# Kernel tuning notes

Hardware: AMD Instinct MI355X
Metric: run time of the kernel (lower is better)

Reference implementation:

```python
import jax, jax.numpy as jnp
import numpy as np

K = 100  # sliding-window size hard-coded in the original forward


def setup_inputs() -> dict:
    key = jax.random.key(0)
    x = jax.random.normal(key, (32, 1, 1124, 1124), dtype=jnp.float32)
    return {"x": x}


def reference(x):
    # Sliding 100x100 mean over every stride-1 patch (gq == patch mean),
    # computed via a 2D integral image (summed-area table) so we never
    # materialize the [B, C, outH, outW, K, K] patch tensor.
    B, C, H, W = x.shape
    s = jnp.cumsum(jnp.cumsum(x, axis=2), axis=3)
    # pad one zero row/col at the front -> S has shape [B, C, H+1, W+1]
    S = jnp.pad(s, ((0, 0), (0, 0), (1, 0), (1, 0)))
    sums = (S[:, :, K:, K:] - S[:, :, :-K, K:]
            - S[:, :, K:, :-K] + S[:, :, :-K, :-K])  # [B, C, H-K+1, W-K+1]
    # gq averages over the whole patch (all channels + spatial) -> 1 channel out
    out = jnp.sum(sums, axis=1, keepdims=True) / jnp.asarray(K * K * C, x.dtype)
    return out  # [B, 1, H-99, W-99]
```

## Files before the change

### kernel.cpp

```cpp
#include <hip/hip_runtime.h>


#define H_IN    1124
#define W_IN    1124
#define KWIN    100
#define W_OUT   1025
#define H_OUT   1025
#define TSTR    1032
#define NBANDS  13
#define BANDR   79

typedef float    f32x4  __attribute__((ext_vector_type(4)));
typedef _Float16 f16x8  __attribute__((ext_vector_type(8)));

__global__ __launch_bounds__(256) void hslide_kernel(
    const float* __restrict__ x,
    _Float16* __restrict__ T)
{
    __shared__ float    srow[W_IN];
    __shared__ float    ps[282];
    __shared__ _Float16 sout[TSTR];

    const int row = blockIdx.x;
    const int tid = threadIdx.x;
    const f32x4* xr4 = (const f32x4*)(x + (size_t)row * W_IN);

    for (int i = tid; i < 281; i += 256)
        ((f32x4*)srow)[i] = __builtin_nontemporal_load(xr4 + i);
    __syncthreads();

    float4 lo = ((const float4*)srow)[tid];
    ps[tid] = lo.x + lo.y + lo.z + lo.w;
    if (tid < 25) {
        float4 v = ((const float4*)srow)[256 + tid];
        ps[256 + tid] = v.x + v.y + v.z + v.w;
    }
    if (tid < 7) sout[1025 + tid] = (_Float16)0.f;
    __syncthreads();

    {
        const int w0 = tid * 4;
        float s = 0.f;
        #pragma unroll
        for (int j = 0; j < 25; ++j) s += ps[tid + j];
        float4 hi = ((const float4*)srow)[tid + 25];
        float s1 = s  + hi.x - lo.x;
        float s2 = s1 + hi.y - lo.y;
        float s3 = s2 + hi.z - lo.z;
        struct alignas(8) hh { _Float16 a, b, c, d; };
        *reinterpret_cast<hh*>(&sout[w0]) =
            hh{ (_Float16)s, (_Float16)s1, (_Float16)s2, (_Float16)s3 };
        if (tid == 255) {
            float t = 0.f;
            #pragma unroll
            for (int j = 0; j < 25; ++j) t += ps[256 + j];
            sout[1024] = (_Float16)t;
        }
    }
    __syncthreads();

    f32x4* tr4 = (f32x4*)(T + (size_t)row * TSTR);
    if (tid < 129) tr4[tid] = ((const f32x4*)sout)[tid];
}

__global__ __launch_bounds__(192) void vslide_kernel(
    const _Float16* __restrict__ T,
    float* __restrict__ out)
{
    const int tid = threadIdx.x;
    if (tid > 128) return;
    const int band = blockIdx.y;
    const int b    = blockIdx.z;
    const int r0   = band * BANDR;
    const int nr   = min(BANDR, H_OUT - r0);
    if (nr <= 0) return;

    const int w0 = tid * 8;
    const _Float16* base = T + ((size_t)b * H_IN + r0) * TSTR + w0;
    const float scale = 1.0f / (float)(KWIN * KWIN);
    const bool full = (tid < 128);

    float s[8];
    #pragma unroll
    for (int j = 0; j < 8; ++j) s[j] = 0.f;

    {
        const _Float16* p = base;
        #pragma unroll 5
        for (int c = 0; c < 25; ++c) {
            f16x8 v0 = *(const f16x8*)(p);
            f16x8 v1 = *(const f16x8*)(p + TSTR);
            f16x8 v2 = *(const f16x8*)(p + 2 * TSTR);
            f16x8 v3 = *(const f16x8*)(p + 3 * TSTR);
            #pragma unroll
            for (int j = 0; j < 8; ++j)
                s[j] += ((float)v0[j] + (float)v1[j])
                      + ((float)v2[j] + (float)v3[j]);
            p += 4 * TSTR;
        }
    }

    float* q = out + ((size_t)b * H_OUT + r0) * W_OUT + w0;

    if (full) {
        #pragma unroll
        for (int j = 0; j < 8; ++j)
            __builtin_nontemporal_store(s[j] * scale, q + j);
    } else {
        __builtin_nontemporal_store(s[0] * scale, q);
    }
    q += W_OUT;

    const _Float16* padd = base + (size_t)KWIN * TSTR;
    const _Float16* psub = base;
    const int steps = nr - 1;
    #pragma unroll 4
    for (int i = 0; i < steps; ++i) {
        f16x8 a = *(const f16x8*)padd;  padd += TSTR;
        f16x8 d = *(const f16x8*)psub;  psub += TSTR;
        #pragma unroll
        for (int j = 0; j < 8; ++j)
            s[j] += (float)a[j] - (float)d[j];
        if (full) {
            #pragma unroll
            for (int j = 0; j < 8; ++j)
                __builtin_nontemporal_store(s[j] * scale, q + j);
        } else {
            __builtin_nontemporal_store(s[0] * scale, q);
        }
        q += W_OUT;
    }
}

extern "C" void kernel_launch(void* const* d_in, const int* in_sizes, int n_in,
                              void* d_out, int out_size, void* d_ws, size_t ws_size,
                              hipStream_t stream) {
    const float* x = (const float*)d_in[0];
    float* out     = (float*)d_out;
    _Float16* ws   = (_Float16*)d_ws;

    const int B = 32;
    const size_t perBatchT = (size_t)H_IN * TSTR * sizeof(_Float16);

    int G = (int)(ws_size / perBatchT);
    if (G > B) G = B;
    if (G < 1) G = 1;

    for (int b0 = 0; b0 < B; b0 += G) {
        const int g = (B - b0 < G) ? (B - b0) : G;

        hslide_kernel<<<g * H_IN, 256, 0, stream>>>(
            x + (size_t)b0 * H_IN * W_IN, ws);

        dim3 vgrid(1, NBANDS, g);
        vslide_kernel<<<vgrid, 192, 0, stream>>>(
            ws, out + (size_t)b0 * H_OUT * W_OUT);
    }
}
```

Baseline: 119.8 us.

## Retile vertical pass into more bands, fold tail column, drop LDS staging

```diff
diff --git a/kernel.cpp b/kernel.cpp
--- a/kernel.cpp
+++ b/kernel.cpp
@@ -7,19 +7,20 @@
 #define W_OUT   1025
 #define H_OUT   1025
 #define TSTR    1032
-#define NBANDS  13
-#define BANDR   79
+#define NBANDS  24
+#define BANDR   43
 
-typedef float    f32x4  __attribute__((ext_vector_type(4)));
-typedef _Float16 f16x8  __attribute__((ext_vector_type(8)));
+typedef float    f32x4 __attribute__((ext_vector_type(4)));
+typedef _Float16 f16x8 __attribute__((ext_vector_type(8)));
+
+struct alignas(8) h4 { _Float16 a, b, c, d; };
 
 __global__ __launch_bounds__(256) void hslide_kernel(
     const float* __restrict__ x,
     _Float16* __restrict__ T)
 {
-    __shared__ float    srow[W_IN];
-    __shared__ float    ps[282];
-    __shared__ _Float16 sout[TSTR];
+    __shared__ float srow[W_IN];
+    __shared__ float ps[282];
 
     const int row = blockIdx.x;
     const int tid = threadIdx.x;
@@ -35,9 +36,9 @@
         float4 v = ((const float4*)srow)[256 + tid];
         ps[256 + tid] = v.x + v.y + v.z + v.w;
     }
-    if (tid < 7) sout[1025 + tid] = (_Float16)0.f;
     __syncthreads();
 
+    _Float16* trow = T + (size_t)row * TSTR;
     {
         const int w0 = tid * 4;
         float s = 0.f;
@@ -47,45 +48,44 @@
         float s1 = s  + hi.x - lo.x;
         float s2 = s1 + hi.y - lo.y;
         float s3 = s2 + hi.z - lo.z;
-        struct alignas(8) hh { _Float16 a, b, c, d; };
-        *reinterpret_cast<hh*>(&sout[w0]) =
-            hh{ (_Float16)s, (_Float16)s1, (_Float16)s2, (_Float16)s3 };
+        *(h4*)(trow + w0) = h4{ (_Float16)s, (_Float16)s1,
+                                (_Float16)s2, (_Float16)s3 };
         if (tid == 255) {
             float t = 0.f;
             #pragma unroll
             for (int j = 0; j < 25; ++j) t += ps[256 + j];
-            sout[1024] = (_Float16)t;
+            *(h4*)(trow + 1024) = h4{ (_Float16)t, (_Float16)0.f,
+                                      (_Float16)0.f, (_Float16)0.f };
+            *(h4*)(trow + 1028) = h4{ (_Float16)0.f, (_Float16)0.f,
+                                      (_Float16)0.f, (_Float16)0.f };
         }
     }
-    __syncthreads();
-
-    f32x4* tr4 = (f32x4*)(T + (size_t)row * TSTR);
-    if (tid < 129) tr4[tid] = ((const f32x4*)sout)[tid];
 }
 
-__global__ __launch_bounds__(192) void vslide_kernel(
+__global__ __launch_bounds__(128) void vslide_kernel(
     const _Float16* __restrict__ T,
     float* __restrict__ out)
 {
-    const int tid = threadIdx.x;
-    if (tid > 128) return;
+    const int tid  = threadIdx.x;
     const int band = blockIdx.y;
     const int b    = blockIdx.z;
     const int r0   = band * BANDR;
     const int nr   = min(BANDR, H_OUT - r0);
-    if (nr <= 0) return;
 
     const int w0 = tid * 8;
-    const _Float16* base = T + ((size_t)b * H_IN + r0) * TSTR + w0;
+    const _Float16* base  = T + ((size_t)b * H_IN + r0) * TSTR + w0;
+    const _Float16* basec = T + ((size_t)b * H_IN + r0) * TSTR + 1024;
+    const bool xtra = (tid == 127);
     const float scale = 1.0f / (float)(KWIN * KWIN);
-    const bool full = (tid < 128);
 
     float s[8];
     #pragma unroll
     for (int j = 0; j < 8; ++j) s[j] = 0.f;
+    float s8 = 0.f;
 
     {
-        const _Float16* p = base;
+        const _Float16* p  = base;
+        const _Float16* pc = basec;
         #pragma unroll 5
         for (int c = 0; c < 25; ++c) {
             f16x8 v0 = *(const f16x8*)(p);
@@ -96,23 +96,24 @@
             for (int j = 0; j < 8; ++j)
                 s[j] += ((float)v0[j] + (float)v1[j])
                       + ((float)v2[j] + (float)v3[j]);
-            p += 4 * TSTR;
+            if (xtra)
+                s8 += ((float)pc[0] + (float)pc[TSTR])
+                    + ((float)pc[2 * TSTR] + (float)pc[3 * TSTR]);
+            p += 4 * TSTR; pc += 4 * TSTR;
         }
     }
 
     float* q = out + ((size_t)b * H_OUT + r0) * W_OUT + w0;
 
-    if (full) {
-        #pragma unroll
-        for (int j = 0; j < 8; ++j)
-            __builtin_nontemporal_store(s[j] * scale, q + j);
-    } else {
-        __builtin_nontemporal_store(s[0] * scale, q);
-    }
+    #pragma unroll
+    for (int j = 0; j < 8; ++j) q[j] = s[j] * scale;
+    if (xtra) q[8] = s8 * scale;
     q += W_OUT;
 
-    const _Float16* padd = base + (size_t)KWIN * TSTR;
-    const _Float16* psub = base;
+    const _Float16* padd  = base  + (size_t)KWIN * TSTR;
+    const _Float16* psub  = base;
+    const _Float16* paddc = basec + (size_t)KWIN * TSTR;
+    const _Float16* psubc = basec;
     const int steps = nr - 1;
     #pragma unroll 4
     for (int i = 0; i < steps; ++i) {
@@ -121,12 +122,12 @@
         #pragma unroll
         for (int j = 0; j < 8; ++j)
             s[j] += (float)a[j] - (float)d[j];
-        if (full) {
-            #pragma unroll
-            for (int j = 0; j < 8; ++j)
-                __builtin_nontemporal_store(s[j] * scale, q + j);
-        } else {
-            __builtin_nontemporal_store(s[0] * scale, q);
+        #pragma unroll
+        for (int j = 0; j < 8; ++j) q[j] = s[j] * scale;
+        if (xtra) {
+            s8 += (float)paddc[0] - (float)psubc[0];
+            paddc += TSTR; psubc += TSTR;
+            q[8] = s8 * scale;
         }
         q += W_OUT;
     }
@@ -153,7 +154,7 @@
             x + (size_t)b0 * H_IN * W_IN, ws);
 
         dim3 vgrid(1, NBANDS, g);
-        vslide_kernel<<<vgrid, 192, 0, stream>>>(
+        vslide_kernel<<<vgrid, 128, 0, stream>>>(
             ws, out + (size_t)b0 * H_OUT * W_OUT);
     }
 }
```

Result: slower. 125.0 us (+4.4%).
